# Optimization experiments

Measured on AMD Instinct MI355X. Metric: run time of the kernel, lower is better.

## Reference

```python
import jax, jax.numpy as jnp
import numpy as np

BIG = 1e6  # sentinel 'no zero pixel found yet' distance; BIG**2 = 1e12 fits fp32


def _edt(is_fg):
    """Exact Euclidean distance transform (scipy.distance_transform_edt semantics):
    distance from each nonzero pixel to the nearest zero pixel. is_fg: [N,H,W] bool.
    Separable exact algorithm: 1D vertical distance-to-zero per column via cummax
    scans, then min-plus convolution with the parabola (j-k)^2 along rows."""
    N, H, W = is_fg.shape
    is_zero = ~is_fg
    ih = jnp.arange(H, dtype=jnp.float32)[None, :, None]
    # nearest zero at-or-above / at-or-below along H (per column)
    up = jax.lax.cummax(jnp.where(is_zero, ih, -BIG), axis=1)
    dn = -jax.lax.cummax(jnp.where(is_zero, -ih, -BIG), axis=1, reverse=True)
    g = jnp.minimum(ih - up, dn - ih)               # [N,H,W] vertical 1D distance
    g2 = jnp.minimum(g, BIG) ** 2
    ks = jnp.arange(W, dtype=jnp.float32)
    def col(j):
        # exact 2D squared distance for output column j: min_k (j-k)^2 + g(.,.,k)^2
        return jnp.min((j.astype(jnp.float32) - ks) ** 2 + g2, axis=-1)  # [N,H]
    d2 = jax.lax.map(col, jnp.arange(W))            # [W,N,H], sequential -> low memory
    return jnp.sqrt(jnp.moveaxis(d2, 0, -1))        # [N,H,W]


def setup_inputs() -> dict:
    key = jax.random.key(0)
    k1, k2 = jax.random.split(key)
    B, C, H, W = 8, 12, 256, 256
    logits = jax.random.normal(k1, (B, C, H, W), dtype=jnp.float32)
    targets = jax.random.randint(k2, (B, H, W), 0, C, dtype=jnp.int32)
    return {"logits": logits, "targets": targets}


def reference(logits, targets):
    B, C, H, W = logits.shape
    probs = jax.nn.softmax(logits, axis=1)                                  # [B,C,H,W]
    gt = targets[:, None, :, :] == jnp.arange(C, dtype=targets.dtype)[None, :, None, None]
    m = gt.reshape(B * C, H, W)
    pos = _edt(m)          # distance inside foreground to nearest background
    neg = _edt(~m)         # distance inside background to nearest foreground
    dt = (neg - pos).reshape(B, C, H, W)
    has_fg = gt.any(axis=(2, 3))                                            # [B,C]
    dt = jnp.where(has_fg[:, :, None, None], dt, 0.0)
    # per-image, per-class min-max normalization (matches torch view(B,-1).min/max)
    dmin = dt.min(axis=(2, 3), keepdims=True)
    dmax = dt.max(axis=(2, 3), keepdims=True)
    dt = (dt - dmin) / (dmax - dmin + 1e-8)
    inter = jnp.sum(probs * dt, axis=(2, 3))                                # [B,C]
    denom = jnp.sum(probs * probs, axis=(2, 3)) + jnp.sum(dt * dt, axis=(2, 3)) + 1e-6
    dice = 2.0 * inter / denom
    # sum_c mean_b (1-dice) / C  == mean over (b,c) since ignore_index=255 is out of range
    return jnp.mean(1.0 - dice)
```

## Files before the change

### kernel.cpp

```cpp
#include <hip/hip_runtime.h>
#include <math.h>

constexpr int B_  = 8;
constexpr int C_  = 12;
constexpr int H_  = 256;
constexpr int W_  = 256;
constexpr int HW_ = H_ * W_;
constexpr int NBC_ = B_ * C_;
constexpr int PAD_ = 256;
constexpr int VB_  = NBC_ * 8;
constexpr int SMB_ = B_ * (HW_ / 1024);


__global__ void __launch_bounds__(256) k_vp(
                     const int* __restrict__ t,
                     const float* __restrict__ logits,
                     unsigned short* __restrict__ gpk,
                     int* __restrict__ hasfg_p,
                     float2* __restrict__ den,
                     float* __restrict__ out) {
    int tid = threadIdx.x;
    if (blockIdx.x >= VB_) {
        int pb = blockIdx.x - VB_;
        int b = pb >> 6;
        int p = ((pb & 63) << 10) + tid * 4;
        const float* lb = logits + (size_t)b * C_ * HW_ + p;
        float4 l[C_];
        float4 mx = make_float4(-3.4e38f, -3.4e38f, -3.4e38f, -3.4e38f);
        #pragma unroll
        for (int c = 0; c < C_; ++c) {
            l[c] = *(const float4*)(lb + (size_t)c * HW_);
            mx.x = fmaxf(mx.x, l[c].x);
            mx.y = fmaxf(mx.y, l[c].y);
            mx.z = fmaxf(mx.z, l[c].z);
            mx.w = fmaxf(mx.w, l[c].w);
        }
        float4 s = make_float4(0.f, 0.f, 0.f, 0.f);
        #pragma unroll
        for (int c = 0; c < C_; ++c) {
            s.x += __expf(l[c].x - mx.x);
            s.y += __expf(l[c].y - mx.y);
            s.z += __expf(l[c].z - mx.z);
            s.w += __expf(l[c].w - mx.w);
        }
        float2* dp = den + (size_t)b * HW_ + p;
        ((float4*)dp)[0] = make_float4(mx.x, 1.0f / s.x, mx.y, 1.0f / s.y);
        ((float4*)dp)[1] = make_float4(mx.z, 1.0f / s.z, mx.w, 1.0f / s.w);
        return;
    }

    if (blockIdx.x == 0 && tid == 0) out[0] = 0.0f;
    constexpr int SEG = 8, SH = 32;
    int s  = tid >> 5;
    int wl = tid & 31;
    int blk = blockIdx.x;
    int bc = blk >> 3;
    int w0 = (blk & 7) * 32;
    int b = bc / C_, c = bc - b * C_;
    int w = w0 + wl;
    const int* base = t + b * HW_ + w;
    int h0 = s * SH;

    unsigned tp[SH / 4];
    int lastEq = -1, lastNeq = -1, firstEq = 256, firstNeq = 256;
    #pragma unroll 8
    for (int i = 0; i < SH; ++i) {
        int tv = base[(h0 + i) * W_];
        if ((i & 3) == 0) tp[i >> 2] = 0;
        tp[i >> 2] |= (unsigned)tv << ((i & 3) * 8);
        int h = h0 + i;
        if (tv == c) { lastEq = h;  if (firstEq  == 256) firstEq  = h; }
        else         { lastNeq = h; if (firstNeq == 256) firstNeq = h; }
    }
    __shared__ int sLE[SEG][32], sLN[SEG][32], sFE[SEG][32], sFN[SEG][32];
    sLE[s][wl] = lastEq; sLN[s][wl] = lastNeq;
    sFE[s][wl] = firstEq; sFN[s][wl] = firstNeq;
    __syncthreads();

    int carLE = -1, carLN = -1;
    for (int q = 0; q < s; ++q) {
        carLE = max(carLE, sLE[q][wl]);
        carLN = max(carLN, sLN[q][wl]);
    }
    int carFE = 256, carFN = 256;
    for (int q = s + 1; q < SEG; ++q) {
        carFE = min(carFE, sFE[q][wl]);
        carFN = min(carFN, sFN[q][wl]);
    }
    bool pred = (s == SEG - 1) && (max(carLE, lastEq) >= 0);
    bool anyfg = __any(pred);
    if (tid == 192) hasfg_p[blk] = anyfg ? 1 : 0;

    int pLE[SH], pLN[SH];
    {
        int le = carLE, ln = carLN;
        #pragma unroll
        for (int i = 0; i < SH; ++i) {
            int tv = (tp[i >> 2] >> ((i & 3) * 8)) & 0xFF;
            int h = h0 + i;
            if (tv == c) le = h; else ln = h;
            pLE[i] = le; pLN[i] = ln;
        }
    }
    {
        int fe = carFE, fn = carFN;
        unsigned short* gk = gpk + (size_t)bc * HW_ + w;
        #pragma unroll
        for (int i = SH - 1; i >= 0; --i) {
            int tv = (tp[i >> 2] >> ((i & 3) * 8)) & 0xFF;
            int h = h0 + i;
            if (tv == c) fe = h; else fn = h;
            bool fg = (tv == c);
            int lastZ = fg ? pLN[i] : pLE[i];
            int nextZ = fg ? fn : fe;
            int dl  = (lastZ < 0)   ? 0x7FFF : (h - lastZ);
            int dnx = (nextZ > 255) ? 0x7FFF : (nextZ - h);
            int d = min(dl, dnx);
            gk[h * W_] = (unsigned short)(d | (fg ? 0x8000 : 0));
        }
    }
}

__global__ void __launch_bounds__(256) k_edt(
                      const unsigned short* __restrict__ gpk,
                      const float* __restrict__ logits,
                      const float2* __restrict__ den,
                      const int* __restrict__ hasfg_p,
                      float* __restrict__ part) {
    __shared__ float sp[4][W_ + 2 * PAD_];
    __shared__ float sn[4][W_ + 2 * PAD_];
    int wave = threadIdx.x >> 6;
    int lane = threadIdx.x & 63;
    int row = blockIdx.x * 4 + wave;
    int bc = row >> 8;
    int b = bc / C_, c = bc - b * C_;
    int h = row & (H_ - 1);

    int hfl = 0;
    if (lane < 8) hfl = hasfg_p[bc * 8 + lane];
    bool hf = __any(hfl != 0);

    float dv[4];
    if (hf) {
        float4 inf4 = make_float4(3.0e38f, 3.0e38f, 3.0e38f, 3.0e38f);
        ((float4*)&sp[wave][0])[lane]          = inf4;
        ((float4*)&sp[wave][PAD_ + W_])[lane]  = inf4;
        ((float4*)&sn[wave][0])[lane]          = inf4;
        ((float4*)&sn[wave][PAD_ + W_])[lane]  = inf4;

        float s1 = (float)(1000000 - h);
        float sent2 = s1 * s1;
        const ushort4 v4 = ((const ushort4*)(gpk + (size_t)row * W_))[lane];
        float4 fpv, fnv;
        {
            const unsigned short* vs = (const unsigned short*)&v4;
            float* fp = (float*)&fpv;
            float* fn = (float*)&fnv;
            #pragma unroll
            for (int q = 0; q < 4; ++q) {
                unsigned v = vs[q];
                unsigned d = v & 0x7FFFu;
                float g2 = (d == 0x7FFFu) ? sent2 : (float)(d * d);
                bool fg = (v & 0x8000u) != 0;
                fp[q] = fg ? g2 : 0.0f;
                fn[q] = fg ? 0.0f : g2;
            }
        }
        ((float4*)&sp[wave][PAD_])[lane] = fpv;
        ((float4*)&sn[wave][PAD_])[lane] = fnv;
        __syncthreads();

        float bp[4], bn[4];
        #pragma unroll
        for (int i = 0; i < 4; ++i) {
            int j = PAD_ + lane + 64 * i;
            bp[i] = sp[wave][j];
            bn[i] = sn[wave][j];
        }
        for (int r = 1; r < W_; ++r) {
            float fr = (float)r;
            float r2 = fr * fr;
            float m = fmaxf(fmaxf(bn[0], bn[1]), fmaxf(bn[2], bn[3]));
            if (!__any(r2 < m)) break;
            #pragma unroll
            for (int i = 0; i < 4; ++i) {
                int j = PAD_ + lane + 64 * i;
                float v = fminf(sn[wave][j - r], sn[wave][j + r]);
                bn[i] = fminf(bn[i], fmaf(fr, fr, v));
            }
        }
        for (int r = 1; r < W_; ++r) {
            float fr = (float)r;
            float r2 = fr * fr;
            float m = fmaxf(fmaxf(bp[0], bp[1]), fmaxf(bp[2], bp[3]));
            if (!__any(r2 < m)) break;
            #pragma unroll
            for (int i = 0; i < 4; ++i) {
                int j = PAD_ + lane + 64 * i;
                float v = fminf(sp[wave][j - r], sp[wave][j + r]);
                bp[i] = fminf(bp[i], fmaf(fr, fr, v));
            }
        }
        #pragma unroll
        for (int i = 0; i < 4; ++i) dv[i] = sqrtf(bn[i]) - sqrtf(bp[i]);
    } else {
        #pragma unroll
        for (int i = 0; i < 4; ++i) dv[i] = 0.0f;
    }

    const float*  lrow = logits + ((size_t)b * C_ + c) * HW_ + h * W_;
    const float2* drow = den + (size_t)b * HW_ + h * W_;
    float s_pd = 0.f, s_p = 0.f, s_pp = 0.f, s_d = 0.f, s_dd = 0.f;
    float mn = 3.4e38f, mx = -3.4e38f;
    #pragma unroll
    for (int i = 0; i < 4; ++i) {
        int j = lane + 64 * i;
        float2 mi = drow[j];
        float pr = __expf(lrow[j] - mi.x) * mi.y;
        float d = dv[i];
        s_pd = fmaf(pr, d, s_pd);
        s_p += pr;
        s_pp = fmaf(pr, pr, s_pp);
        s_d += d;
        s_dd = fmaf(d, d, s_dd);
        mn = fminf(mn, d);
        mx = fmaxf(mx, d);
    }
    #pragma unroll
    for (int off = 32; off; off >>= 1) {
        s_pd += __shfl_down(s_pd, off);
        s_p  += __shfl_down(s_p, off);
        s_pp += __shfl_down(s_pp, off);
        s_d  += __shfl_down(s_d, off);
        s_dd += __shfl_down(s_dd, off);
        mn = fminf(mn, __shfl_down(mn, off));
        mx = fmaxf(mx, __shfl_down(mx, off));
    }
    if (lane == 0) {
        float* p8 = part + (size_t)row * 8;
        p8[0] = s_pd; p8[1] = s_p; p8[2] = s_pp;
        p8[3] = s_d;  p8[4] = s_dd; p8[5] = mn; p8[6] = mx;
    }
}

__global__ void __launch_bounds__(256) k_bcred(
                       const float* __restrict__ part, float* __restrict__ out) {
    int bc = blockIdx.x;
    int tid = threadIdx.x;
    const float* p8 = part + ((size_t)bc * 256 + tid) * 8;
    float s_pd = p8[0], s_p = p8[1], s_pp = p8[2];
    float s_d = p8[3], s_dd = p8[4], mn = p8[5], mx = p8[6];
    #pragma unroll
    for (int off = 32; off; off >>= 1) {
        s_pd += __shfl_down(s_pd, off);
        s_p  += __shfl_down(s_p, off);
        s_pp += __shfl_down(s_pp, off);
        s_d  += __shfl_down(s_d, off);
        s_dd += __shfl_down(s_dd, off);
        mn = fminf(mn, __shfl_down(mn, off));
        mx = fmaxf(mx, __shfl_down(mx, off));
    }
    __shared__ float red[4][7];
    int wave = tid >> 6, lane = tid & 63;
    if (lane == 0) {
        red[wave][0] = s_pd; red[wave][1] = s_p; red[wave][2] = s_pp;
        red[wave][3] = s_d;  red[wave][4] = s_dd; red[wave][5] = mn; red[wave][6] = mx;
    }
    __syncthreads();
    if (tid == 0) {
        s_pd = red[0][0]; s_p = red[0][1]; s_pp = red[0][2];
        s_d = red[0][3]; s_dd = red[0][4]; mn = red[0][5]; mx = red[0][6];
        for (int w = 1; w < 4; ++w) {
            s_pd += red[w][0]; s_p += red[w][1]; s_pp += red[w][2];
            s_d += red[w][3]; s_dd += red[w][4];
            mn = fminf(mn, red[w][5]); mx = fmaxf(mx, red[w][6]);
        }
        float sc = 1.0f / (mx - mn + 1e-8f);
        float inter = sc * (s_pd - mn * s_p);
        float d2 = sc * sc * (s_dd - 2.0f * mn * s_d + mn * mn * (float)HW_);
        float dice = 2.0f * inter / (s_pp + d2 + 1e-6f);
        atomicAdd(out, (1.0f - dice) * (1.0f / (float)NBC_));
    }
}

extern "C" void kernel_launch(void* const* d_in, const int* in_sizes, int n_in,
                              void* d_out, int out_size, void* d_ws, size_t ws_size,
                              hipStream_t stream) {
    const float* logits  = (const float*)d_in[0];
    const int*   targets = (const int*)d_in[1];
    float* out = (float*)d_out;

    unsigned short* gpk = (unsigned short*)d_ws;
    int* hasfg_p = (int*)(gpk + (size_t)NBC_ * HW_);
    float* part = (float*)(hasfg_p + NBC_ * 8);
    float2* den = (float2*)(part + (size_t)NBC_ * H_ * 8);

    k_vp<<<VB_ + SMB_, 256, 0, stream>>>(targets, logits, gpk,
                                         hasfg_p, den, out);
    k_edt<<<NBC_ * H_ / 4, 256, 0, stream>>>(gpk, logits, den, hasfg_p, part);
    k_bcred<<<NBC_, 256, 0, stream>>>(part, out);
}
```

Measured before the change: 107.4 us.

## Process two columns per thread in vertical pass and prefetch logits in EDT kernel

The vertical-distance kernel now handles two adjacent columns per thread, using int2 loads and packed 32-bit stores. This halves the block count and swaps the per-row int arrays for byte-packed last-zero offsets to cut register pressure. The EDT kernel issues its logits and softmax-denominator loads before the row distance transform so their latency overlaps it. It also replaces the block-wide barrier with a wave-local LDS wait, which is valid because each wave only touches its own shared rows. Fewer, heavier vertical blocks may reduce parallelism, and the hasfg reduction layout changes to four entries per class.

```diff
diff --git a/kernel.cpp b/kernel.cpp
--- a/kernel.cpp
+++ b/kernel.cpp
@@ -8,7 +8,7 @@
 constexpr int HW_ = H_ * W_;
 constexpr int NBC_ = B_ * C_;
 constexpr int PAD_ = 256;
-constexpr int VB_  = NBC_ * 8;
+constexpr int VB_  = NBC_ * 4;
 constexpr int SMB_ = B_ * (HW_ / 1024);
 
 
@@ -54,69 +54,100 @@
     int s  = tid >> 5;
     int wl = tid & 31;
     int blk = blockIdx.x;
-    int bc = blk >> 3;
-    int w0 = (blk & 7) * 32;
+    int bc = blk >> 2;
+    int w0 = (blk & 3) * 64;
     int b = bc / C_, c = bc - b * C_;
-    int w = w0 + wl;
+    int w = w0 + 2 * wl;
     const int* base = t + b * HW_ + w;
     int h0 = s * SH;
 
-    unsigned tp[SH / 4];
-    int lastEq = -1, lastNeq = -1, firstEq = 256, firstNeq = 256;
-    #pragma unroll 8
+    unsigned tp0[SH / 4], tp1[SH / 4];
+    int le0 = -1, ln0 = -1, fe0 = 256, fn0 = 256;
+    int le1 = -1, ln1 = -1, fe1 = 256, fn1 = 256;
+    #pragma unroll
     for (int i = 0; i < SH; ++i) {
-        int tv = base[(h0 + i) * W_];
-        if ((i & 3) == 0) tp[i >> 2] = 0;
-        tp[i >> 2] |= (unsigned)tv << ((i & 3) * 8);
+        int2 tv = *(const int2*)(base + (h0 + i) * W_);
+        if ((i & 3) == 0) { tp0[i >> 2] = 0; tp1[i >> 2] = 0; }
+        tp0[i >> 2] |= (unsigned)tv.x << ((i & 3) * 8);
+        tp1[i >> 2] |= (unsigned)tv.y << ((i & 3) * 8);
         int h = h0 + i;
-        if (tv == c) { lastEq = h;  if (firstEq  == 256) firstEq  = h; }
-        else         { lastNeq = h; if (firstNeq == 256) firstNeq = h; }
-    }
-    __shared__ int sLE[SEG][32], sLN[SEG][32], sFE[SEG][32], sFN[SEG][32];
-    sLE[s][wl] = lastEq; sLN[s][wl] = lastNeq;
-    sFE[s][wl] = firstEq; sFN[s][wl] = firstNeq;
+        if (tv.x == c) { le0 = h; if (fe0 == 256) fe0 = h; }
+        else           { ln0 = h; if (fn0 == 256) fn0 = h; }
+        if (tv.y == c) { le1 = h; if (fe1 == 256) fe1 = h; }
+        else           { ln1 = h; if (fn1 == 256) fn1 = h; }
+    }
+    __shared__ int sLE[SEG][64], sLN[SEG][64], sFE[SEG][64], sFN[SEG][64];
+    sLE[s][2 * wl] = le0; sLE[s][2 * wl + 1] = le1;
+    sLN[s][2 * wl] = ln0; sLN[s][2 * wl + 1] = ln1;
+    sFE[s][2 * wl] = fe0; sFE[s][2 * wl + 1] = fe1;
+    sFN[s][2 * wl] = fn0; sFN[s][2 * wl + 1] = fn1;
     __syncthreads();
 
-    int carLE = -1, carLN = -1;
+    int carLE0 = -1, carLN0 = -1, carLE1 = -1, carLN1 = -1;
     for (int q = 0; q < s; ++q) {
-        carLE = max(carLE, sLE[q][wl]);
-        carLN = max(carLN, sLN[q][wl]);
-    }
-    int carFE = 256, carFN = 256;
+        carLE0 = max(carLE0, sLE[q][2 * wl]);
+        carLN0 = max(carLN0, sLN[q][2 * wl]);
+        carLE1 = max(carLE1, sLE[q][2 * wl + 1]);
+        carLN1 = max(carLN1, sLN[q][2 * wl + 1]);
+    }
+    int carFE0 = 256, carFN0 = 256, carFE1 = 256, carFN1 = 256;
     for (int q = s + 1; q < SEG; ++q) {
-        carFE = min(carFE, sFE[q][wl]);
-        carFN = min(carFN, sFN[q][wl]);
-    }
-    bool pred = (s == SEG - 1) && (max(carLE, lastEq) >= 0);
+        carFE0 = min(carFE0, sFE[q][2 * wl]);
+        carFN0 = min(carFN0, sFN[q][2 * wl]);
+        carFE1 = min(carFE1, sFE[q][2 * wl + 1]);
+        carFN1 = min(carFN1, sFN[q][2 * wl + 1]);
+    }
+
+    bool pred = false;
+    if (tid < 64) {
+        int m = -1;
+        #pragma unroll
+        for (int q = 0; q < SEG; ++q) m = max(m, sLE[q][tid]);
+        pred = (m >= 0);
+    }
     bool anyfg = __any(pred);
-    if (tid == 192) hasfg_p[blk] = anyfg ? 1 : 0;
-
-    int pLE[SH], pLN[SH];
+    if (tid == 0) hasfg_p[blk] = anyfg ? 1 : 0;
+
+    unsigned ap0[SH / 4], ap1[SH / 4];
     {
-        int le = carLE, ln = carLN;
+        int l0 = carLE0, n0 = carLN0, l1 = carLE1, n1 = carLN1;
         #pragma unroll
         for (int i = 0; i < SH; ++i) {
-            int tv = (tp[i >> 2] >> ((i & 3) * 8)) & 0xFF;
             int h = h0 + i;
-            if (tv == c) le = h; else ln = h;
-            pLE[i] = le; pLN[i] = ln;
+            int tv0 = (tp0[i >> 2] >> ((i & 3) * 8)) & 0xFF;
+            int tv1 = (tp1[i >> 2] >> ((i & 3) * 8)) & 0xFF;
+            int lz0, lz1;
+            if (tv0 == c) { l0 = h; lz0 = n0; } else { n0 = h; lz0 = l0; }
+            if (tv1 == c) { l1 = h; lz1 = n1; } else { n1 = h; lz1 = l1; }
+            unsigned a0 = (lz0 < 0) ? 255u : (unsigned)(h - lz0 - 1);
+            unsigned a1 = (lz1 < 0) ? 255u : (unsigned)(h - lz1 - 1);
+            if ((i & 3) == 0) { ap0[i >> 2] = 0; ap1[i >> 2] = 0; }
+            ap0[i >> 2] |= a0 << ((i & 3) * 8);
+            ap1[i >> 2] |= a1 << ((i & 3) * 8);
         }
     }
     {
-        int fe = carFE, fn = carFN;
-        unsigned short* gk = gpk + (size_t)bc * HW_ + w;
+        int fe0_ = carFE0, fn0_ = carFN0, fe1_ = carFE1, fn1_ = carFN1;
+        unsigned* gk32 = (unsigned*)(gpk + (size_t)bc * HW_ + w);
         #pragma unroll
         for (int i = SH - 1; i >= 0; --i) {
-            int tv = (tp[i >> 2] >> ((i & 3) * 8)) & 0xFF;
             int h = h0 + i;
-            if (tv == c) fe = h; else fn = h;
-            bool fg = (tv == c);
-            int lastZ = fg ? pLN[i] : pLE[i];
-            int nextZ = fg ? fn : fe;
-            int dl  = (lastZ < 0)   ? 0x7FFF : (h - lastZ);
-            int dnx = (nextZ > 255) ? 0x7FFF : (nextZ - h);
-            int d = min(dl, dnx);
-            gk[h * W_] = (unsigned short)(d | (fg ? 0x8000 : 0));
+            int tv0 = (tp0[i >> 2] >> ((i & 3) * 8)) & 0xFF;
+            int tv1 = (tp1[i >> 2] >> ((i & 3) * 8)) & 0xFF;
+            int nz0, nz1; bool fg0, fg1;
+            if (tv0 == c) { fe0_ = h; fg0 = true;  nz0 = fn0_; }
+            else          { fn0_ = h; fg0 = false; nz0 = fe0_; }
+            if (tv1 == c) { fe1_ = h; fg1 = true;  nz1 = fn1_; }
+            else          { fn1_ = h; fg1 = false; nz1 = fe1_; }
+            unsigned au0 = (ap0[i >> 2] >> ((i & 3) * 8)) & 0xFF;
+            unsigned au1 = (ap1[i >> 2] >> ((i & 3) * 8)) & 0xFF;
+            int dl0 = (au0 == 255u) ? 0x7FFF : (int)au0 + 1;
+            int dl1 = (au1 == 255u) ? 0x7FFF : (int)au1 + 1;
+            int dn0 = (nz0 > 255) ? 0x7FFF : (nz0 - h);
+            int dn1 = (nz1 > 255) ? 0x7FFF : (nz1 - h);
+            unsigned d0 = (unsigned)min(dl0, dn0) | (fg0 ? 0x8000u : 0u);
+            unsigned d1 = (unsigned)min(dl1, dn1) | (fg1 ? 0x8000u : 0u);
+            gk32[(h * W_) >> 1] = d0 | (d1 << 16);
         }
     }
 }
@@ -137,11 +168,23 @@
     int h = row & (H_ - 1);
 
     int hfl = 0;
-    if (lane < 8) hfl = hasfg_p[bc * 8 + lane];
+    if (lane < 4) hfl = hasfg_p[bc * 4 + lane];
     bool hf = __any(hfl != 0);
+
+    const float*  lrow = logits + ((size_t)b * C_ + c) * HW_ + h * W_;
+    const float2* drow = den + (size_t)b * HW_ + h * W_;
+    float lv[4]; float2 mv[4];
+    #pragma unroll
+    for (int i = 0; i < 4; ++i) {
+        int j = lane + 64 * i;
+        lv[i] = lrow[j];
+        mv[i] = drow[j];
+    }
 
     float dv[4];
     if (hf) {
+        const ushort4 v4 = ((const ushort4*)(gpk + (size_t)row * W_))[lane];
+
         float4 inf4 = make_float4(3.0e38f, 3.0e38f, 3.0e38f, 3.0e38f);
         ((float4*)&sp[wave][0])[lane]          = inf4;
         ((float4*)&sp[wave][PAD_ + W_])[lane]  = inf4;
@@ -150,7 +193,6 @@
 
         float s1 = (float)(1000000 - h);
         float sent2 = s1 * s1;
-        const ushort4 v4 = ((const ushort4*)(gpk + (size_t)row * W_))[lane];
         float4 fpv, fnv;
         {
             const unsigned short* vs = (const unsigned short*)&v4;
@@ -168,7 +210,7 @@
         }
         ((float4*)&sp[wave][PAD_])[lane] = fpv;
         ((float4*)&sn[wave][PAD_])[lane] = fnv;
-        __syncthreads();
+        asm volatile("s_waitcnt lgkmcnt(0)" ::: "memory");
 
         float bp[4], bn[4];
         #pragma unroll
@@ -208,15 +250,12 @@
         for (int i = 0; i < 4; ++i) dv[i] = 0.0f;
     }
 
-    const float*  lrow = logits + ((size_t)b * C_ + c) * HW_ + h * W_;
-    const float2* drow = den + (size_t)b * HW_ + h * W_;
     float s_pd = 0.f, s_p = 0.f, s_pp = 0.f, s_d = 0.f, s_dd = 0.f;
     float mn = 3.4e38f, mx = -3.4e38f;
     #pragma unroll
     for (int i = 0; i < 4; ++i) {
-        int j = lane + 64 * i;
-        float2 mi = drow[j];
-        float pr = __expf(lrow[j] - mi.x) * mi.y;
+        float2 mi = mv[i];
+        float pr = __expf(lv[i] - mi.x) * mi.y;
         float d = dv[i];
         s_pd = fmaf(pr, d, s_pd);
         s_p += pr;
```

Result: slower. 109.7 us (+2.1%).
